# Kernel tuning notes

Measured on AMD Instinct MI355X. Metric: run time of the kernel, lower is better.

Reference implementation:

```python
import jax, jax.numpy as jnp
import numpy as np


def setup_inputs() -> dict:
    key = jax.random.key(0)
    ks = jax.random.split(key, 4)
    d, d_k, d_v = 1024, 128, 128
    B, S = 4, 4096
    scale = 1.0 / np.sqrt(d)
    return {
        "X": jax.random.normal(ks[0], (B, S, d), dtype=jnp.float32),
        "W_q": jax.random.normal(ks[1], (d, d_k), dtype=jnp.float32) * scale,
        "b_q": jnp.zeros((d_k,), dtype=jnp.float32),
        "W_k": jax.random.normal(ks[2], (d, d_k), dtype=jnp.float32) * scale,
        "b_k": jnp.zeros((d_k,), dtype=jnp.float32),
        "W_v": jax.random.normal(ks[3], (d, d_v), dtype=jnp.float32) * scale,
        "b_v": jnp.zeros((d_v,), dtype=jnp.float32),
    }


def reference(X, W_q, b_q, W_k, b_k, W_v, b_v):
    # Projections: [B, S, d_k/d_v]
    Q = jnp.einsum("bsd,dk->bsk", X, W_q) + b_q
    K = jnp.einsum("bsd,dk->bsk", X, W_k) + b_k
    V = jnp.einsum("bsd,dv->bsv", X, W_v) + b_v

    d_k = Q.shape[-1]
    # Scaled dot-product scores: [B, S, S]
    scores = jnp.einsum("bqk,bsk->bqs", Q, K) / jnp.sqrt(jnp.float32(d_k))
    # Causal (lower-triangular) mask
    S = scores.shape[-1]
    causal = jnp.tril(jnp.ones((S, S), dtype=bool))
    scores = jnp.where(causal[None, :, :], scores, -jnp.inf)
    weights = jax.nn.softmax(scores, axis=-1)
    # Weighted sum of values: [B, S, d_v]
    return jnp.einsum("bqs,bsv->bqv", weights, V)
```

## Files before the change

### kernel.cpp

```cpp
#include <hip/hip_runtime.h>
#include <hip/hip_bf16.h>
#include <stdint.h>


typedef __bf16 bf16x8 __attribute__((ext_vector_type(8)));
typedef float  f32x4  __attribute__((ext_vector_type(4)));
typedef unsigned int u32x4 __attribute__((ext_vector_type(4)));
typedef unsigned int u32x2 __attribute__((ext_vector_type(2)));

using bf16 = __hip_bfloat16;

#define AS1 __attribute__((address_space(1)))
#define AS3 __attribute__((address_space(3)))

__device__ __forceinline__ void gl_lds16(const void* g, void* l) {
  __builtin_amdgcn_global_load_lds((AS1 uint32_t*)g, (AS3 uint32_t*)l, 16, 0, 0);
}

__global__ __launch_bounds__(256) void k_wt(const float* __restrict__ Wq,
                                            const float* __restrict__ Wk,
                                            const float* __restrict__ Wv,
                                            bf16* __restrict__ Wt) {
  __shared__ bf16 t[64][72];
  const float* W = blockIdx.z == 0 ? Wq : (blockIdx.z == 1 ? Wk : Wv);
  int k0 = blockIdx.x * 64, n0 = blockIdx.y * 64;
  int tid = threadIdx.x;
  int r = tid >> 4, c4 = (tid & 15) * 4;
#pragma unroll
  for (int s = 0; s < 4; ++s) {
    int rr = r + s * 16;
    float4 v = *(const float4*)(W + (size_t)(k0 + rr) * 128 + n0 + c4);
    t[rr][c4 + 0] = __float2bfloat16(v.x);
    t[rr][c4 + 1] = __float2bfloat16(v.y);
    t[rr][c4 + 2] = __float2bfloat16(v.z);
    t[rr][c4 + 3] = __float2bfloat16(v.w);
  }
  __syncthreads();
  bf16* out = Wt + (size_t)blockIdx.z * 128 * 1024;
#pragma unroll
  for (int s = 0; s < 4; ++s) {
    int rn = r + s * 16;
    union { bf16 h[4]; u32x2 v; } u;
    u.h[0] = t[c4 + 0][rn]; u.h[1] = t[c4 + 1][rn];
    u.h[2] = t[c4 + 2][rn]; u.h[3] = t[c4 + 3][rn];
    *(u32x2*)(out + (size_t)(n0 + rn) * 1024 + k0 + c4) = u.v;
  }
}

__global__ __launch_bounds__(512) void k_qkv(const float* __restrict__ X,
                                             const bf16* __restrict__ Wt,
                                             const float* __restrict__ bq,
                                             const float* __restrict__ bk,
                                             const float* __restrict__ bv,
                                             bf16* __restrict__ Qo,
                                             bf16* __restrict__ Ko,
                                             bf16* __restrict__ Vt) {
  __shared__ __align__(16) char smem[65536];
  float* Xs = (float*)smem;
  bf16* Ws = (bf16*)(smem + 16384);
  bf16* Vs = (bf16*)smem;

  const int m0 = blockIdx.x * 64;
  const int tid = threadIdx.x;
  const int lane = tid & 63;
  const int li = lane & 15, g = lane >> 4;
  const int wid = tid >> 6;
  const int wm = wid >> 2, wn = wid & 3;

  const int xr = tid >> 3;
  const int xc32 = (tid & 7) >> 1;
  const int xhf = tid & 1;
  const int wr = tid >> 2;
  const int wc = tid & 3;

  f32x4 acc[3][2][2] = {};

  {
    gl_lds16(X + (size_t)(m0 + xr) * 1024 + (xc32 ^ (xr & 3)) * 8 + xhf * 4,
             Xs + tid * 4);
#pragma unroll
    for (int z = 0; z < 3; ++z)
      gl_lds16(Wt + (size_t)z * 131072 + (size_t)wr * 1024 + (wc ^ (wr & 3)) * 8,
               Ws + z * 4096 + tid * 8);
  }
  int cur = 0;
  for (int kt = 0; kt < 32; ++kt) {
    __syncthreads();
    if (kt < 31) {
      const int k0 = (kt + 1) * 32;
      gl_lds16(X + (size_t)(m0 + xr) * 1024 + k0 + (xc32 ^ (xr & 3)) * 8 + xhf * 4,
               Xs + (cur ^ 1) * 2048 + tid * 4);
#pragma unroll
      for (int z = 0; z < 3; ++z)
        gl_lds16(Wt + (size_t)z * 131072 + (size_t)wr * 1024 + k0 + (wc ^ (wr & 3)) * 8,
                 Ws + (cur ^ 1) * 12288 + z * 4096 + tid * 8);
    }
    bf16x8 af[2];
#pragma unroll
    for (int mf = 0; mf < 2; ++mf) {
      int r = wm * 32 + mf * 16 + li;
      const float* xp = Xs + cur * 2048 + r * 32 + ((g ^ (r & 3)) * 8);
      f32x4 x0 = *(const f32x4*)xp;
      f32x4 x1 = *(const f32x4*)(xp + 4);
      union { bf16 h[8]; bf16x8 v; } u;
      u.h[0] = __float2bfloat16(x0[0]); u.h[1] = __float2bfloat16(x0[1]);
      u.h[2] = __float2bfloat16(x0[2]); u.h[3] = __float2bfloat16(x0[3]);
      u.h[4] = __float2bfloat16(x1[0]); u.h[5] = __float2bfloat16(x1[1]);
      u.h[6] = __float2bfloat16(x1[2]); u.h[7] = __float2bfloat16(x1[3]);
      af[mf] = u.v;
    }
#pragma unroll
    for (int z = 0; z < 3; ++z) {
#pragma unroll
      for (int nf = 0; nf < 2; ++nf) {
        int r = wn * 32 + nf * 16 + li;
        bf16x8 bfrag =
            *(const bf16x8*)(Ws + cur * 12288 + z * 4096 + r * 32 + ((g ^ (r & 3)) * 8));
#pragma unroll
        for (int mf = 0; mf < 2; ++mf)
          acc[z][mf][nf] = __builtin_amdgcn_mfma_f32_16x16x32_bf16(
              af[mf], bfrag, acc[z][mf][nf], 0, 0, 0);
      }
    }
    cur ^= 1;
  }

#pragma unroll
  for (int z = 0; z < 2; ++z) {
    const float* bias = z == 0 ? bq : bk;
    bf16* Out = z == 0 ? Qo : Ko;
    const float scale = z == 0 ? 0.12752404368678202f : 1.0f;
#pragma unroll
    for (int nf = 0; nf < 2; ++nf) {
      int col = wn * 32 + nf * 16 + li;
      float bb = bias[col];
#pragma unroll
      for (int mf = 0; mf < 2; ++mf)
#pragma unroll
        for (int j = 0; j < 4; ++j) {
          int row = m0 + wm * 32 + mf * 16 + g * 4 + j;
          Out[(size_t)row * 128 + col] =
              __float2bfloat16((acc[z][mf][nf][j] + bb) * scale);
        }
    }
  }

  __syncthreads();
#pragma unroll
  for (int nf = 0; nf < 2; ++nf) {
    int col = wn * 32 + nf * 16 + li;
    float bb = bv[col];
#pragma unroll
    for (int mf = 0; mf < 2; ++mf)
#pragma unroll
      for (int j = 0; j < 4; ++j) {
        int row = wm * 32 + mf * 16 + g * 4 + j;
        Vs[row * 136 + col] = __float2bfloat16(acc[2][mf][nf][j] + bb);
      }
  }
  __syncthreads();
  const int b = m0 >> 12;
  const int s_off = m0 & 4095;
#pragma unroll
  for (int t2 = 0; t2 < 2; ++t2) {
    int idx = tid + 512 * t2;
    int dv = idx & 127;
    int sg = idx >> 7;
    union { bf16 h[8]; u32x4 v; } u;
#pragma unroll
    for (int si = 0; si < 8; ++si) u.h[si] = Vs[(sg * 8 + si) * 136 + dv];
    *(u32x4*)(Vt + (size_t)(b * 128 + dv) * 4096 + s_off + sg * 8) = u.v;
  }
}

__global__ __launch_bounds__(256, 2) void k_attn(const bf16* __restrict__ Qb,
                                                 const bf16* __restrict__ Kb,
                                                 const bf16* __restrict__ Vt,
                                                 bf16* __restrict__ o_part,
                                                 float* __restrict__ l_part) {
  __shared__ __align__(16) bf16 Kls[2][64 * 128];
  __shared__ __align__(16) bf16 Vls[2][128 * 64];
  __shared__ __align__(16) bf16 Pls[4][32 * 36];

  const int bid = blockIdx.x;
  const int xcd = bid & 7;
  const int slot = xcd * 72 + (bid >> 3);
  const int b = slot / 144;
  const int s = 143 - (slot - b * 144);
  const int widx = b * 144 + s;
  int qt = 0;
#pragma unroll
  for (int q2 = 1; q2 < 32; ++q2) {
    int M = q2 >> 2;
    if ((M + 1) * (2 * M + (q2 & 3)) <= s) qt = q2;
  }
  const int Mq = qt >> 2;
  const int chunk = s - (Mq + 1) * (2 * Mq + (qt & 3));
  const int ntiles = 2 * qt + 2;
  const int nch = (qt + 4) >> 2;
  const int clen = ntiles / nch;
  const int crem = ntiles - clen * nch;
  const int kt0 = chunk * clen + min(chunk, crem);
  const int kt1 = kt0 + clen + (chunk < crem ? 1 : 0) - 1;

  const int tid = threadIdx.x;
  const int lane = tid & 63;
  const int li = lane & 15, g = lane >> 4;
  const int w = tid >> 6;

  bf16x8 qf[2][4];
#pragma unroll
  for (int qb = 0; qb < 2; ++qb)
#pragma unroll
    for (int ks = 0; ks < 4; ++ks)
      qf[qb][ks] = *(const bf16x8*)(Qb +
          (size_t)(b * 4096 + qt * 128 + w * 32 + qb * 16 + li) * 128 +
          ks * 32 + g * 8);

  f32x4 o[2][8] = {};
  f32x4 lacc[2] = {};
  bf16x8 ones;
#pragma unroll
  for (int e = 0; e < 8; ++e) ones[e] = (__bf16)1.0f;

  bf16* P = &Pls[w][0];
  const bf16* Vtb = Vt + (size_t)b * 128 * 4096;

  {
    const int kv0 = kt0 * 64;
#pragma unroll
    for (int ii = 0; ii < 4; ++ii) {
      int c = tid + 256 * ii;
      int r = c >> 4, cc = c & 15;
      gl_lds16(Kb + (size_t)(b * 4096 + kv0 + r) * 128 + (cc ^ (r & 7)) * 8,
               &Kls[0][c * 8]);
      int r2 = c >> 3, cc2 = c & 7;
      gl_lds16(Vtb + (size_t)r2 * 4096 + kv0 + (cc2 ^ (r2 & 7)) * 8,
               &Vls[0][c * 8]);
    }
  }
  int cur = 0;
  for (int kt = kt0; kt <= kt1; ++kt) {
    __syncthreads();
    if (kt < kt1) {
      const int kv0n = (kt + 1) * 64;
#pragma unroll
      for (int ii = 0; ii < 4; ++ii) {
        int c = tid + 256 * ii;
        int r = c >> 4, cc = c & 15;
        gl_lds16(Kb + (size_t)(b * 4096 + kv0n + r) * 128 + (cc ^ (r & 7)) * 8,
                 &Kls[cur ^ 1][c * 8]);
        int r2 = c >> 3, cc2 = c & 7;
        gl_lds16(Vtb + (size_t)r2 * 4096 + kv0n + (cc2 ^ (r2 & 7)) * 8,
                 &Vls[cur ^ 1][c * 8]);
      }
    }
    const bf16* Kl = &Kls[cur][0];
    const bf16* Vl = &Vls[cur][0];
    const int kv0 = kt * 64;

    f32x4 st[2][4] = {};
#pragma unroll
    for (int ks = 0; ks < 4; ++ks) {
      bf16x8 kf[4];
#pragma unroll
      for (int nf = 0; nf < 4; ++nf) {
        int r = nf * 16 + li;
        int ch = (ks * 4 + g) ^ (r & 7);
        kf[nf] = *(const bf16x8*)(Kl + r * 128 + ch * 8);
      }
#pragma unroll
      for (int nf = 0; nf < 4; ++nf)
#pragma unroll
        for (int qb = 0; qb < 2; ++qb)
          st[qb][nf] = __builtin_amdgcn_mfma_f32_16x16x32_bf16(
              kf[nf], qf[qb][ks], st[qb][nf], 0, 0, 0);
    }

    if (kt >= 2 * qt) {
      const int dk = kv0 - qt * 128;
#pragma unroll
      for (int qb = 0; qb < 2; ++qb) {
        const int qloc = w * 32 + qb * 16 + li;
#pragma unroll
        for (int nf = 0; nf < 4; ++nf)
#pragma unroll
          for (int j = 0; j < 4; ++j)
            if (dk + nf * 16 + g * 4 + j > qloc) st[qb][nf][j] = -1e30f;
      }
    }

#pragma unroll
    for (int h = 0; h < 2; ++h) {
#pragma unroll
      for (int qb = 0; qb < 2; ++qb)
#pragma unroll
        for (int nfh = 0; nfh < 2; ++nfh) {
          const f32x4 sv = st[qb][h * 2 + nfh];
          union { bf16 h4[4]; u32x2 v; } u;
#pragma unroll
          for (int j = 0; j < 4; ++j)
            u.h4[j] = __float2bfloat16(exp2f(sv[j]));
          *(u32x2*)(P + (qb * 16 + li) * 36 + nfh * 16 + g * 4) = u.v;
        }
      bf16x8 pa[2];
#pragma unroll
      for (int qb = 0; qb < 2; ++qb)
        pa[qb] = *(const bf16x8*)(P + (qb * 16 + li) * 36 + g * 8);
#pragma unroll
      for (int dvf = 0; dvf < 8; ++dvf) {
        int r = dvf * 16 + li;
        int ch = (h * 4 + g) ^ (li & 7);
        bf16x8 vf = *(const bf16x8*)(Vl + r * 64 + ch * 8);
#pragma unroll
        for (int qb = 0; qb < 2; ++qb)
          o[qb][dvf] = __builtin_amdgcn_mfma_f32_16x16x32_bf16(
              vf, pa[qb], o[qb][dvf], 0, 0, 0);
      }
#pragma unroll
      for (int qb = 0; qb < 2; ++qb)
        lacc[qb] = __builtin_amdgcn_mfma_f32_16x16x32_bf16(
            ones, pa[qb], lacc[qb], 0, 0, 0);
    }
    cur ^= 1;
  }

  bf16* op = o_part + (size_t)widx * (128 * 128);
  float* lp = l_part + widx * 128;
#pragma unroll
  for (int qb = 0; qb < 2; ++qb) {
    const int qloc = w * 32 + qb * 16 + li;
    if (g == 0) lp[qloc] = lacc[qb][0];
#pragma unroll
    for (int dvf = 0; dvf < 8; ++dvf) {
      union { bf16 h4[4]; u32x2 v; } u;
#pragma unroll
      for (int j = 0; j < 4; ++j) u.h4[j] = __float2bfloat16(o[qb][dvf][j]);
      *(u32x2*)(op + (size_t)qloc * 128 + dvf * 16 + g * 4) = u.v;
    }
  }
}

__global__ __launch_bounds__(256) void k_comb(const bf16* __restrict__ op,
                                              const float* __restrict__ lp,
                                              float* __restrict__ out) {
  int i = blockIdx.x * 256 + threadIdx.x;
  int row = i >> 5;
  int col4 = (i & 31) * 4;
  int b = row >> 12;
  int rb = row & 4095;
  int qt = rb >> 7;
  int lr = rb & 127;
  int M = qt >> 2;
  int base = b * 144 + (M + 1) * (2 * M + (qt & 3));
  int n = (qt + 4) >> 2;
  float l = 0.0f;
  float acc0 = 0, acc1 = 0, acc2 = 0, acc3 = 0;
  for (int c = 0; c < n; ++c) {
    l += lp[(base + c) * 128 + lr];
    union { bf16 h[4]; u32x2 v; } u;
    u.v = *(const u32x2*)(op + (size_t)(base + c) * 16384 + lr * 128 + col4);
    acc0 += __bfloat162float(u.h[0]);
    acc1 += __bfloat162float(u.h[1]);
    acc2 += __bfloat162float(u.h[2]);
    acc3 += __bfloat162float(u.h[3]);
  }
  float linv = 1.0f / l;
  float4 rv;
  rv.x = acc0 * linv; rv.y = acc1 * linv; rv.z = acc2 * linv; rv.w = acc3 * linv;
  ((float4*)out)[i] = rv;
}

extern "C" void kernel_launch(void* const* d_in, const int* in_sizes, int n_in,
                              void* d_out, int out_size, void* d_ws, size_t ws_size,
                              hipStream_t stream) {
  const float* X  = (const float*)d_in[0];
  const float* Wq = (const float*)d_in[1];
  const float* bq = (const float*)d_in[2];
  const float* Wk = (const float*)d_in[3];
  const float* bk = (const float*)d_in[4];
  const float* Wv = (const float*)d_in[5];
  const float* bv = (const float*)d_in[6];
  float* out = (float*)d_out;

  char* ws = (char*)d_ws;
  bf16* Wt  = (bf16*)(ws + 0);
  bf16* Qb  = (bf16*)(ws + 786432);
  bf16* Kb  = (bf16*)(ws + 4980736);
  bf16* Vt  = (bf16*)(ws + 9175040);
  bf16* o_part = (bf16*)(ws + 13369344);
  float* l_part = (float*)(ws + 32243712);

  k_wt<<<dim3(16, 2, 3), dim3(256), 0, stream>>>(Wq, Wk, Wv, Wt);
  k_qkv<<<dim3(256), dim3(512), 0, stream>>>(X, Wt, bq, bk, bv, Qb, Kb, Vt);
  k_attn<<<dim3(576), dim3(256), 0, stream>>>(Qb, Kb, Vt, o_part, l_part);
  k_comb<<<dim3(2048), dim3(256), 0, stream>>>(o_part, l_part, out);
}
```

Baseline: 89.75 us.

## Drop K/V LDS double buffering in attention kernel to raise occupancy to three blocks

Replaces the double-buffered K/V shared-memory tiles with single buffers, so each tile is loaded and synchronized before compute and a second barrier follows compute. LDS per block roughly halves and launch bounds move from 2 to 3 blocks per CU, so other resident blocks can hide memory latency in place of in-block prefetch. In exchange, global-to-LDS loads no longer overlap compute within a block, an extra barrier is added per tile, and the register budget is tighter.

```diff
diff --git a/kernel.cpp b/kernel.cpp
--- a/kernel.cpp
+++ b/kernel.cpp
@@ -173,13 +173,13 @@
   }
 }
 
-__global__ __launch_bounds__(256, 2) void k_attn(const bf16* __restrict__ Qb,
+__global__ __launch_bounds__(256, 3) void k_attn(const bf16* __restrict__ Qb,
                                                  const bf16* __restrict__ Kb,
                                                  const bf16* __restrict__ Vt,
                                                  bf16* __restrict__ o_part,
                                                  float* __restrict__ l_part) {
-  __shared__ __align__(16) bf16 Kls[2][64 * 128];
-  __shared__ __align__(16) bf16 Vls[2][128 * 64];
+  __shared__ __align__(16) bf16 Kls[64 * 128];
+  __shared__ __align__(16) bf16 Vls[128 * 64];
   __shared__ __align__(16) bf16 Pls[4][32 * 36];
 
   const int bid = blockIdx.x;
@@ -226,38 +226,19 @@
   bf16* P = &Pls[w][0];
   const bf16* Vtb = Vt + (size_t)b * 128 * 4096;
 
-  {
-    const int kv0 = kt0 * 64;
+  for (int kt = kt0; kt <= kt1; ++kt) {
+    const int kv0 = kt * 64;
 #pragma unroll
     for (int ii = 0; ii < 4; ++ii) {
       int c = tid + 256 * ii;
       int r = c >> 4, cc = c & 15;
       gl_lds16(Kb + (size_t)(b * 4096 + kv0 + r) * 128 + (cc ^ (r & 7)) * 8,
-               &Kls[0][c * 8]);
+               &Kls[c * 8]);
       int r2 = c >> 3, cc2 = c & 7;
       gl_lds16(Vtb + (size_t)r2 * 4096 + kv0 + (cc2 ^ (r2 & 7)) * 8,
-               &Vls[0][c * 8]);
-    }
-  }
-  int cur = 0;
-  for (int kt = kt0; kt <= kt1; ++kt) {
+               &Vls[c * 8]);
+    }
     __syncthreads();
-    if (kt < kt1) {
-      const int kv0n = (kt + 1) * 64;
-#pragma unroll
-      for (int ii = 0; ii < 4; ++ii) {
-        int c = tid + 256 * ii;
-        int r = c >> 4, cc = c & 15;
-        gl_lds16(Kb + (size_t)(b * 4096 + kv0n + r) * 128 + (cc ^ (r & 7)) * 8,
-                 &Kls[cur ^ 1][c * 8]);
-        int r2 = c >> 3, cc2 = c & 7;
-        gl_lds16(Vtb + (size_t)r2 * 4096 + kv0n + (cc2 ^ (r2 & 7)) * 8,
-                 &Vls[cur ^ 1][c * 8]);
-      }
-    }
-    const bf16* Kl = &Kls[cur][0];
-    const bf16* Vl = &Vls[cur][0];
-    const int kv0 = kt * 64;
 
     f32x4 st[2][4] = {};
 #pragma unroll
@@ -267,7 +248,7 @@
       for (int nf = 0; nf < 4; ++nf) {
         int r = nf * 16 + li;
         int ch = (ks * 4 + g) ^ (r & 7);
-        kf[nf] = *(const bf16x8*)(Kl + r * 128 + ch * 8);
+        kf[nf] = *(const bf16x8*)(Kls + r * 128 + ch * 8);
       }
 #pragma unroll
       for (int nf = 0; nf < 4; ++nf)
@@ -311,7 +292,7 @@
       for (int dvf = 0; dvf < 8; ++dvf) {
         int r = dvf * 16 + li;
         int ch = (h * 4 + g) ^ (li & 7);
-        bf16x8 vf = *(const bf16x8*)(Vl + r * 64 + ch * 8);
+        bf16x8 vf = *(const bf16x8*)(Vls + r * 64 + ch * 8);
 #pragma unroll
         for (int qb = 0; qb < 2; ++qb)
           o[qb][dvf] = __builtin_amdgcn_mfma_f32_16x16x32_bf16(
@@ -322,7 +303,7 @@
         lacc[qb] = __builtin_amdgcn_mfma_f32_16x16x32_bf16(
             ones, pa[qb], lacc[qb], 0, 0, 0);
     }
-    cur ^= 1;
+    __syncthreads();
   }
 
   bf16* op = o_part + (size_t)widx * (128 * 128);
```

Result: slower. 97.73 us (+8.9%).

## Split attention work across 8 waves with 16 query rows each

Applied to the files above, without the earlier changes.

The attention kernel now launches 512 threads (8 waves) per block, with each wave owning 16 query rows instead of 32. This halves the per-wave Q fragments, score and output accumulators, lowering register pressure and doubling the waves available to hide latency. The K/V tile loads are spread over more threads. In exchange, each K and V fragment read from LDS is reused by only one MFMA per wave instead of two, which raises LDS read traffic per unit of compute. The launch bound also requests higher occupancy, which may force register limits.

```diff
diff --git a/kernel.cpp b/kernel.cpp
--- a/kernel.cpp
+++ b/kernel.cpp
@@ -173,14 +173,14 @@
   }
 }
 
-__global__ __launch_bounds__(256, 2) void k_attn(const bf16* __restrict__ Qb,
+__global__ __launch_bounds__(512, 4) void k_attn(const bf16* __restrict__ Qb,
                                                  const bf16* __restrict__ Kb,
                                                  const bf16* __restrict__ Vt,
                                                  bf16* __restrict__ o_part,
                                                  float* __restrict__ l_part) {
   __shared__ __align__(16) bf16 Kls[2][64 * 128];
   __shared__ __align__(16) bf16 Vls[2][128 * 64];
-  __shared__ __align__(16) bf16 Pls[4][32 * 36];
+  __shared__ __align__(16) bf16 Pls[8][16 * 36];
 
   const int bid = blockIdx.x;
   const int xcd = bid & 7;
@@ -206,31 +206,28 @@
   const int tid = threadIdx.x;
   const int lane = tid & 63;
   const int li = lane & 15, g = lane >> 4;
-  const int w = tid >> 6;
-
-  bf16x8 qf[2][4];
-#pragma unroll
-  for (int qb = 0; qb < 2; ++qb)
-#pragma unroll
-    for (int ks = 0; ks < 4; ++ks)
-      qf[qb][ks] = *(const bf16x8*)(Qb +
-          (size_t)(b * 4096 + qt * 128 + w * 32 + qb * 16 + li) * 128 +
-          ks * 32 + g * 8);
-
-  f32x4 o[2][8] = {};
-  f32x4 lacc[2] = {};
+  const int w8 = tid >> 6;
+
+  bf16x8 qf[4];
+#pragma unroll
+  for (int ks = 0; ks < 4; ++ks)
+    qf[ks] = *(const bf16x8*)(Qb +
+        (size_t)(b * 4096 + qt * 128 + w8 * 16 + li) * 128 + ks * 32 + g * 8);
+
+  f32x4 o[8] = {};
+  f32x4 lacc = {};
   bf16x8 ones;
 #pragma unroll
   for (int e = 0; e < 8; ++e) ones[e] = (__bf16)1.0f;
 
-  bf16* P = &Pls[w][0];
+  bf16* P = &Pls[w8][0];
   const bf16* Vtb = Vt + (size_t)b * 128 * 4096;
 
   {
     const int kv0 = kt0 * 64;
 #pragma unroll
-    for (int ii = 0; ii < 4; ++ii) {
-      int c = tid + 256 * ii;
+    for (int ii = 0; ii < 2; ++ii) {
+      int c = tid + 512 * ii;
       int r = c >> 4, cc = c & 15;
       gl_lds16(Kb + (size_t)(b * 4096 + kv0 + r) * 128 + (cc ^ (r & 7)) * 8,
                &Kls[0][c * 8]);
@@ -245,8 +242,8 @@
     if (kt < kt1) {
       const int kv0n = (kt + 1) * 64;
 #pragma unroll
-      for (int ii = 0; ii < 4; ++ii) {
-        int c = tid + 256 * ii;
+      for (int ii = 0; ii < 2; ++ii) {
+        int c = tid + 512 * ii;
         int r = c >> 4, cc = c & 15;
         gl_lds16(Kb + (size_t)(b * 4096 + kv0n + r) * 128 + (cc ^ (r & 7)) * 8,
                  &Kls[cur ^ 1][c * 8]);
@@ -259,7 +256,7 @@
     const bf16* Vl = &Vls[cur][0];
     const int kv0 = kt * 64;
 
-    f32x4 st[2][4] = {};
+    f32x4 st[4] = {};
 #pragma unroll
     for (int ks = 0; ks < 4; ++ks) {
       bf16x8 kf[4];
@@ -271,71 +268,55 @@
       }
 #pragma unroll
       for (int nf = 0; nf < 4; ++nf)
-#pragma unroll
-        for (int qb = 0; qb < 2; ++qb)
-          st[qb][nf] = __builtin_amdgcn_mfma_f32_16x16x32_bf16(
-              kf[nf], qf[qb][ks], st[qb][nf], 0, 0, 0);
+        st[nf] = __builtin_amdgcn_mfma_f32_16x16x32_bf16(
+            kf[nf], qf[ks], st[nf], 0, 0, 0);
     }
 
     if (kt >= 2 * qt) {
       const int dk = kv0 - qt * 128;
-#pragma unroll
-      for (int qb = 0; qb < 2; ++qb) {
-        const int qloc = w * 32 + qb * 16 + li;
-#pragma unroll
-        for (int nf = 0; nf < 4; ++nf)
-#pragma unroll
-          for (int j = 0; j < 4; ++j)
-            if (dk + nf * 16 + g * 4 + j > qloc) st[qb][nf][j] = -1e30f;
-      }
+      const int qloc = w8 * 16 + li;
+#pragma unroll
+      for (int nf = 0; nf < 4; ++nf)
+#pragma unroll
+        for (int j = 0; j < 4; ++j)
+          if (dk + nf * 16 + g * 4 + j > qloc) st[nf][j] = -1e30f;
     }
 
 #pragma unroll
     for (int h = 0; h < 2; ++h) {
 #pragma unroll
-      for (int qb = 0; qb < 2; ++qb)
-#pragma unroll
-        for (int nfh = 0; nfh < 2; ++nfh) {
-          const f32x4 sv = st[qb][h * 2 + nfh];
-          union { bf16 h4[4]; u32x2 v; } u;
-#pragma unroll
-          for (int j = 0; j < 4; ++j)
-            u.h4[j] = __float2bfloat16(exp2f(sv[j]));
-          *(u32x2*)(P + (qb * 16 + li) * 36 + nfh * 16 + g * 4) = u.v;
-        }
-      bf16x8 pa[2];
-#pragma unroll
-      for (int qb = 0; qb < 2; ++qb)
-        pa[qb] = *(const bf16x8*)(P + (qb * 16 + li) * 36 + g * 8);
+      for (int nfh = 0; nfh < 2; ++nfh) {
+        const f32x4 sv = st[h * 2 + nfh];
+        union { bf16 h4[4]; u32x2 v; } u;
+#pragma unroll
+        for (int j = 0; j < 4; ++j)
+          u.h4[j] = __float2bfloat16(exp2f(sv[j]));
+        *(u32x2*)(P + li * 36 + nfh * 16 + g * 4) = u.v;
+      }
+      bf16x8 pa = *(const bf16x8*)(P + li * 36 + g * 8);
 #pragma unroll
       for (int dvf = 0; dvf < 8; ++dvf) {
         int r = dvf * 16 + li;
         int ch = (h * 4 + g) ^ (li & 7);
         bf16x8 vf = *(const bf16x8*)(Vl + r * 64 + ch * 8);
-#pragma unroll
-        for (int qb = 0; qb < 2; ++qb)
-          o[qb][dvf] = __builtin_amdgcn_mfma_f32_16x16x32_bf16(
-              vf, pa[qb], o[qb][dvf], 0, 0, 0);
-      }
-#pragma unroll
-      for (int qb = 0; qb < 2; ++qb)
-        lacc[qb] = __builtin_amdgcn_mfma_f32_16x16x32_bf16(
-            ones, pa[qb], lacc[qb], 0, 0, 0);
+        o[dvf] = __builtin_amdgcn_mfma_f32_16x16x32_bf16(
+            vf, pa, o[dvf], 0, 0, 0);
+      }
+      lacc = __builtin_amdgcn_mfma_f32_16x16x32_bf16(ones, pa, lacc, 0, 0, 0);
     }
     cur ^= 1;
   }
 
   bf16* op = o_part + (size_t)widx * (128 * 128);
   float* lp = l_part + widx * 128;
-#pragma unroll
-  for (int qb = 0; qb < 2; ++qb) {
-    const int qloc = w * 32 + qb * 16 + li;
-    if (g == 0) lp[qloc] = lacc[qb][0];
+  {
+    const int qloc = w8 * 16 + li;
+    if (g == 0) lp[qloc] = lacc[0];
 #pragma unroll
     for (int dvf = 0; dvf < 8; ++dvf) {
       union { bf16 h4[4]; u32x2 v; } u;
 #pragma unroll
-      for (int j = 0; j < 4; ++j) u.h4[j] = __float2bfloat16(o[qb][dvf][j]);
+      for (int j = 0; j < 4; ++j) u.h4[j] = __float2bfloat16(o[dvf][j]);
       *(u32x2*)(op + (size_t)qloc * 128 + dvf * 16 + g * 4) = u.v;
     }
   }
@@ -393,6 +374,6 @@
 
   k_wt<<<dim3(16, 2, 3), dim3(256), 0, stream>>>(Wq, Wk, Wv, Wt);
   k_qkv<<<dim3(256), dim3(512), 0, stream>>>(X, Wt, bq, bk, bv, Qb, Kb, Vt);
-  k_attn<<<dim3(576), dim3(256), 0, stream>>>(Qb, Kb, Vt, o_part, l_part);
+  k_attn<<<dim3(576), dim3(512), 0, stream>>>(Qb, Kb, Vt, o_part, l_part);
   k_comb<<<dim3(2048), dim3(256), 0, stream>>>(o_part, l_part, out);
 }
```

Measured after the change: 87.84 us. 2.1% less time.

## Halve attention query tile to 64 rows and split keys across warp pairs

Applied to the files above, without the earlier changes.

The attention kernel now processes 64-query tiles, with KV chunks of up to eight 64-key tiles, and launches twice as many blocks. Within a block, two warp pairs each take 32 queries and split every key tile between two warps. Partial outputs are summed through LDS at the end. The combine kernel's indexing is updated to match. The aim is to cut causal-mask waste and improve load balance and occupancy. In exchange it adds an LDS reduction step, writes more partials, and gives each warp less MFMA work per K/V load.

```diff
diff --git a/kernel.cpp b/kernel.cpp
--- a/kernel.cpp
+++ b/kernel.cpp
@@ -178,35 +178,34 @@
                                                  const bf16* __restrict__ Vt,
                                                  bf16* __restrict__ o_part,
                                                  float* __restrict__ l_part) {
-  __shared__ __align__(16) bf16 Kls[2][64 * 128];
-  __shared__ __align__(16) bf16 Vls[2][128 * 64];
-  __shared__ __align__(16) bf16 Pls[4][32 * 36];
+  __shared__ __align__(16) char smem[74752];
+  bf16* Kls0 = (bf16*)smem;
+  bf16* Vls0 = (bf16*)(smem + 32768);
+  bf16* Pls  = (bf16*)(smem + 65536);
+  f32x4* xch = (f32x4*)smem;
 
   const int bid = blockIdx.x;
-  const int xcd = bid & 7;
-  const int slot = xcd * 72 + (bid >> 3);
-  const int b = slot / 144;
-  const int s = 143 - (slot - b * 144);
-  const int widx = b * 144 + s;
-  int qt = 0;
-#pragma unroll
-  for (int q2 = 1; q2 < 32; ++q2) {
-    int M = q2 >> 2;
-    if ((M + 1) * (2 * M + (q2 & 3)) <= s) qt = q2;
-  }
-  const int Mq = qt >> 2;
-  const int chunk = s - (Mq + 1) * (2 * Mq + (qt & 3));
-  const int ntiles = 2 * qt + 2;
-  const int nch = (qt + 4) >> 2;
-  const int clen = ntiles / nch;
-  const int crem = ntiles - clen * nch;
-  const int kt0 = chunk * clen + min(chunk, crem);
-  const int kt1 = kt0 + clen + (chunk < crem ? 1 : 0) - 1;
+  const int slot = (bid & 7) * 144 + (bid >> 3);
+  const int b = slot / 288;
+  const int s = 287 - (slot - b * 288);
+  const int widx = b * 288 + s;
+  int kgrp = 0;
+#pragma unroll
+  for (int kk = 1; kk < 8; ++kk)
+    if (4 * kk * (kk + 1) <= s) kgrp = kk;
+  const int t = s - 4 * kgrp * (kgrp + 1);
+  const int tq = t / (kgrp + 1);
+  const int qt = 8 * kgrp + tq;
+  const int chunk = t - tq * (kgrp + 1);
+  const int kt0 = chunk * 8;
+  const int kt1 = min(kt0 + 7, qt);
 
   const int tid = threadIdx.x;
   const int lane = tid & 63;
   const int li = lane & 15, g = lane >> 4;
   const int w = tid >> 6;
+  const int qg = w >> 1;
+  const int h = w & 1;
 
   bf16x8 qf[2][4];
 #pragma unroll
@@ -214,7 +213,7 @@
 #pragma unroll
     for (int ks = 0; ks < 4; ++ks)
       qf[qb][ks] = *(const bf16x8*)(Qb +
-          (size_t)(b * 4096 + qt * 128 + w * 32 + qb * 16 + li) * 128 +
+          (size_t)(b * 4096 + qt * 64 + qg * 32 + qb * 16 + li) * 128 +
           ks * 32 + g * 8);
 
   f32x4 o[2][8] = {};
@@ -223,7 +222,7 @@
 #pragma unroll
   for (int e = 0; e < 8; ++e) ones[e] = (__bf16)1.0f;
 
-  bf16* P = &Pls[w][0];
+  bf16* P = Pls + w * 1152;
   const bf16* Vtb = Vt + (size_t)b * 128 * 4096;
 
   {
@@ -233,10 +232,10 @@
       int c = tid + 256 * ii;
       int r = c >> 4, cc = c & 15;
       gl_lds16(Kb + (size_t)(b * 4096 + kv0 + r) * 128 + (cc ^ (r & 7)) * 8,
-               &Kls[0][c * 8]);
+               Kls0 + c * 8);
       int r2 = c >> 3, cc2 = c & 7;
       gl_lds16(Vtb + (size_t)r2 * 4096 + kv0 + (cc2 ^ (r2 & 7)) * 8,
-               &Vls[0][c * 8]);
+               Vls0 + c * 8);
     }
   }
   int cur = 0;
@@ -249,94 +248,112 @@
         int c = tid + 256 * ii;
         int r = c >> 4, cc = c & 15;
         gl_lds16(Kb + (size_t)(b * 4096 + kv0n + r) * 128 + (cc ^ (r & 7)) * 8,
-                 &Kls[cur ^ 1][c * 8]);
+                 Kls0 + (cur ^ 1) * 8192 + c * 8);
         int r2 = c >> 3, cc2 = c & 7;
         gl_lds16(Vtb + (size_t)r2 * 4096 + kv0n + (cc2 ^ (r2 & 7)) * 8,
-                 &Vls[cur ^ 1][c * 8]);
-      }
-    }
-    const bf16* Kl = &Kls[cur][0];
-    const bf16* Vl = &Vls[cur][0];
-    const int kv0 = kt * 64;
-
-    f32x4 st[2][4] = {};
+                 Vls0 + (cur ^ 1) * 8192 + c * 8);
+      }
+    }
+    const bf16* Kl = Kls0 + cur * 8192;
+    const bf16* Vl = Vls0 + cur * 8192;
+
+    f32x4 st[2][2] = {};
 #pragma unroll
     for (int ks = 0; ks < 4; ++ks) {
-      bf16x8 kf[4];
-#pragma unroll
-      for (int nf = 0; nf < 4; ++nf) {
-        int r = nf * 16 + li;
+      bf16x8 kf[2];
+#pragma unroll
+      for (int nf = 0; nf < 2; ++nf) {
+        int r = h * 32 + nf * 16 + li;
         int ch = (ks * 4 + g) ^ (r & 7);
         kf[nf] = *(const bf16x8*)(Kl + r * 128 + ch * 8);
       }
 #pragma unroll
-      for (int nf = 0; nf < 4; ++nf)
+      for (int nf = 0; nf < 2; ++nf)
 #pragma unroll
         for (int qb = 0; qb < 2; ++qb)
           st[qb][nf] = __builtin_amdgcn_mfma_f32_16x16x32_bf16(
               kf[nf], qf[qb][ks], st[qb][nf], 0, 0, 0);
     }
 
-    if (kt >= 2 * qt) {
-      const int dk = kv0 - qt * 128;
+    if (kt == qt) {
 #pragma unroll
       for (int qb = 0; qb < 2; ++qb) {
-        const int qloc = w * 32 + qb * 16 + li;
-#pragma unroll
-        for (int nf = 0; nf < 4; ++nf)
+        const int qloc = qg * 32 + qb * 16 + li;
+#pragma unroll
+        for (int nf = 0; nf < 2; ++nf)
 #pragma unroll
           for (int j = 0; j < 4; ++j)
-            if (dk + nf * 16 + g * 4 + j > qloc) st[qb][nf][j] = -1e30f;
-      }
-    }
-
-#pragma unroll
-    for (int h = 0; h < 2; ++h) {
+            if (h * 32 + nf * 16 + g * 4 + j > qloc) st[qb][nf][j] = -1e30f;
+      }
+    }
+
+#pragma unroll
+    for (int qb = 0; qb < 2; ++qb)
+#pragma unroll
+      for (int nf = 0; nf < 2; ++nf) {
+        const f32x4 sv = st[qb][nf];
+        union { bf16 h4[4]; u32x2 v; } u;
+#pragma unroll
+        for (int j = 0; j < 4; ++j)
+          u.h4[j] = __float2bfloat16(exp2f(sv[j]));
+        *(u32x2*)(P + (qb * 16 + li) * 36 + nf * 16 + g * 4) = u.v;
+      }
+    bf16x8 pa[2];
+#pragma unroll
+    for (int qb = 0; qb < 2; ++qb)
+      pa[qb] = *(const bf16x8*)(P + (qb * 16 + li) * 36 + g * 8);
+#pragma unroll
+    for (int dvf = 0; dvf < 8; ++dvf) {
+      int r = dvf * 16 + li;
+      int ch = (h * 4 + g) ^ (li & 7);
+      bf16x8 vf = *(const bf16x8*)(Vl + r * 64 + ch * 8);
 #pragma unroll
       for (int qb = 0; qb < 2; ++qb)
-#pragma unroll
-        for (int nfh = 0; nfh < 2; ++nfh) {
-          const f32x4 sv = st[qb][h * 2 + nfh];
-          union { bf16 h4[4]; u32x2 v; } u;
-#pragma unroll
-          for (int j = 0; j < 4; ++j)
-            u.h4[j] = __float2bfloat16(exp2f(sv[j]));
-          *(u32x2*)(P + (qb * 16 + li) * 36 + nfh * 16 + g * 4) = u.v;
-        }
-      bf16x8 pa[2];
-#pragma unroll
-      for (int qb = 0; qb < 2; ++qb)
-        pa[qb] = *(const bf16x8*)(P + (qb * 16 + li) * 36 + g * 8);
+        o[qb][dvf] = __builtin_amdgcn_mfma_f32_16x16x32_bf16(
+            vf, pa[qb], o[qb][dvf], 0, 0, 0);
+    }
+#pragma unroll
+    for (int qb = 0; qb < 2; ++qb)
+      lacc[qb] = __builtin_amdgcn_mfma_f32_16x16x32_bf16(
+          ones, pa[qb], lacc[qb], 0, 0, 0);
+    cur ^= 1;
+  }
+
+  __syncthreads();
+  if (h == 1) {
+    f32x4* xw = xch + qg * (18 * 64) + lane;
+#pragma unroll
+    for (int qb = 0; qb < 2; ++qb)
+#pragma unroll
+      for (int dvf = 0; dvf < 8; ++dvf)
+        xw[(qb * 8 + dvf) * 64] = o[qb][dvf];
+    xw[16 * 64] = lacc[0];
+    xw[17 * 64] = lacc[1];
+  }
+  __syncthreads();
+  if (h == 0) {
+    const f32x4* xr = xch + qg * (18 * 64) + lane;
+#pragma unroll
+    for (int qb = 0; qb < 2; ++qb)
+#pragma unroll
+      for (int dvf = 0; dvf < 8; ++dvf)
+        o[qb][dvf] += xr[(qb * 8 + dvf) * 64];
+    lacc[0] += xr[16 * 64];
+    lacc[1] += xr[17 * 64];
+
+    bf16* op = o_part + (size_t)widx * (64 * 128);
+    float* lp = l_part + widx * 64;
+#pragma unroll
+    for (int qb = 0; qb < 2; ++qb) {
+      const int qloc = qg * 32 + qb * 16 + li;
+      if (g == 0) lp[qloc] = lacc[qb][0];
 #pragma unroll
       for (int dvf = 0; dvf < 8; ++dvf) {
-        int r = dvf * 16 + li;
-        int ch = (h * 4 + g) ^ (li & 7);
-        bf16x8 vf = *(const bf16x8*)(Vl + r * 64 + ch * 8);
-#pragma unroll
-        for (int qb = 0; qb < 2; ++qb)
-          o[qb][dvf] = __builtin_amdgcn_mfma_f32_16x16x32_bf16(
-              vf, pa[qb], o[qb][dvf], 0, 0, 0);
-      }
-#pragma unroll
-      for (int qb = 0; qb < 2; ++qb)
-        lacc[qb] = __builtin_amdgcn_mfma_f32_16x16x32_bf16(
-            ones, pa[qb], lacc[qb], 0, 0, 0);
-    }
-    cur ^= 1;
-  }
-
-  bf16* op = o_part + (size_t)widx * (128 * 128);
-  float* lp = l_part + widx * 128;
-#pragma unroll
-  for (int qb = 0; qb < 2; ++qb) {
-    const int qloc = w * 32 + qb * 16 + li;
-    if (g == 0) lp[qloc] = lacc[qb][0];
-#pragma unroll
-    for (int dvf = 0; dvf < 8; ++dvf) {
-      union { bf16 h4[4]; u32x2 v; } u;
-#pragma unroll
-      for (int j = 0; j < 4; ++j) u.h4[j] = __float2bfloat16(o[qb][dvf][j]);
-      *(u32x2*)(op + (size_t)qloc * 128 + dvf * 16 + g * 4) = u.v;
+        union { bf16 h4[4]; u32x2 v; } u;
+#pragma unroll
+        for (int j = 0; j < 4; ++j) u.h4[j] = __float2bfloat16(o[qb][dvf][j]);
+        *(u32x2*)(op + (size_t)qloc * 128 + dvf * 16 + g * 4) = u.v;
+      }
     }
   }
 }
@@ -349,17 +366,17 @@
   int col4 = (i & 31) * 4;
   int b = row >> 12;
   int rb = row & 4095;
-  int qt = rb >> 7;
-  int lr = rb & 127;
-  int M = qt >> 2;
-  int base = b * 144 + (M + 1) * (2 * M + (qt & 3));
-  int n = (qt + 4) >> 2;
+  int qt = rb >> 6;
+  int lr = rb & 63;
+  int a = qt >> 3, r = qt & 7;
+  int base = b * 288 + (a + 1) * (4 * a + r);
+  int n = a + 1;
   float l = 0.0f;
   float acc0 = 0, acc1 = 0, acc2 = 0, acc3 = 0;
   for (int c = 0; c < n; ++c) {
-    l += lp[(base + c) * 128 + lr];
+    l += lp[(base + c) * 64 + lr];
     union { bf16 h[4]; u32x2 v; } u;
-    u.v = *(const u32x2*)(op + (size_t)(base + c) * 16384 + lr * 128 + col4);
+    u.v = *(const u32x2*)(op + (size_t)(base + c) * 8192 + lr * 128 + col4);
     acc0 += __bfloat162float(u.h[0]);
     acc1 += __bfloat162float(u.h[1]);
     acc2 += __bfloat162float(u.h[2]);
@@ -393,6 +410,6 @@
 
   k_wt<<<dim3(16, 2, 3), dim3(256), 0, stream>>>(Wq, Wk, Wv, Wt);
   k_qkv<<<dim3(256), dim3(512), 0, stream>>>(X, Wt, bq, bk, bv, Qb, Kb, Vt);
-  k_attn<<<dim3(576), dim3(256), 0, stream>>>(Qb, Kb, Vt, o_part, l_part);
+  k_attn<<<dim3(1152), dim3(256), 0, stream>>>(Qb, Kb, Vt, o_part, l_part);
   k_comb<<<dim3(2048), dim3(256), 0, stream>>>(o_part, l_part, out);
 }
```

After: 91.71 us. +2.2%, slower.
